# Kernel tuning notes

Hardware: AMD Instinct MI355X
Metric: run time of the kernel (lower is better)

Reference implementation:

```python
import jax, jax.numpy as jnp
import numpy as np

B, S, D = 64, 256, 512          # batch, seq_len_max, num_dim (= in_dim = nclass)
H, DO = 8, 64                   # num_heads, out_dim per head (H*DO == D)
ALPHA = 0.2                     # leaky_relu negative slope
N = B * S                       # nodes
DEG = 32
E = N * DEG + N                 # random edges + self-loops


def setup_inputs() -> dict:
    key = jax.random.key(0)
    k = jax.random.split(key, 7)
    h = jax.random.normal(k[0], (B, S, D), jnp.float32)
    loops = jnp.arange(N, dtype=jnp.int32)
    src = jnp.concatenate([jax.random.randint(k[1], (N * DEG,), 0, N, jnp.int32), loops])
    dst = jnp.concatenate([jax.random.randint(k[2], (N * DEG,), 0, N, jnp.int32), loops])
    W1 = jax.random.normal(k[3], (H, D, DO), jnp.float32) * 0.05      # per-head fc weight
    a1 = jax.random.normal(k[4], (H, 2 * DO), jnp.float32) * 0.05     # per-head attn_fc weight
    Wout = jax.random.normal(k[5], (H * DO, D), jnp.float32) * 0.05   # out_att fc
    aout = jax.random.normal(k[6], (2 * D,), jnp.float32) * 0.05      # out_att attn_fc
    return {"h": h, "W1": W1, "a1": a1, "Wout": Wout, "aout": aout, "src": src, "dst": dst}


def gat_head(x, W, a, src, dst, concat):
    # x: [N, in_d], W: [in_d, d], a: [2d]
    z = x @ W                                   # [N, d]
    d = W.shape[1]
    es = z @ a[:d]                              # src part of attn score, [N]
    ed = z @ a[d:]                              # dst part, [N]
    e = jax.nn.leaky_relu(es[src] + ed[dst], ALPHA)   # [E]
    # segment softmax over incoming edges of each dst node
    m = jax.ops.segment_max(e, dst, num_segments=N)
    m = jnp.where(jnp.isfinite(m), m, 0.0)
    ex = jnp.exp(e - m[dst])
    den = jax.ops.segment_sum(ex, dst, num_segments=N)
    att = ex / den[dst]                         # [E] (self-loops guarantee den > 0)
    out = jax.ops.segment_sum(att[:, None] * z[src], dst, num_segments=N)  # [N, d]
    return jax.nn.elu(out) if concat else out


def reference(h, W1, a1, Wout, aout, src, dst):
    x = h.reshape(N, D)                         # dropout is identity at eval
    heads = jax.vmap(lambda W, a: gat_head(x, W, a, src, dst, True))(W1, a1)  # [H, N, DO]
    hcat = jnp.transpose(heads, (1, 0, 2)).reshape(N, H * DO)                 # [N, H*DO]
    out = jax.nn.elu(gat_head(hcat, Wout, aout, src, dst, False))             # [N, D]
    return (out + x).reshape(B, S, D)
```

## Files before the change

kernel.cpp:

```cpp
#include <hip/hip_runtime.h>
#include <stdint.h>

#define DD 512
#define HH 8
#define DOO 64
#define ALPHA 0.2f

typedef __attribute__((ext_vector_type(8))) short short8;
typedef __attribute__((ext_vector_type(4))) float floatx4;
typedef __attribute__((ext_vector_type(4))) unsigned short u16x4;
typedef unsigned short u16;

static __device__ __forceinline__ float bf2f(u16 u){
  union { unsigned int u; float f; } c; c.u = ((unsigned int)u) << 16; return c.f;
}
static __device__ __forceinline__ u16 f2bf(float f){
  union { float f; unsigned int u; } c; c.f = f;
  unsigned int u = c.u;
  unsigned int r = (u + 0x7FFFu + ((u >> 16) & 1u)) >> 16;
  return (u16)r;
}
static __device__ __forceinline__ float leaky(float s){ return (s >= 0.f) ? s : ALPHA * s; }
static __device__ __forceinline__ float elu(float v){ return (v > 0.f) ? v : (__expf(v) - 1.f); }

#define PERM_LO 0x01000504u
#define PERM_HI 0x03020706u

#define DOT2(accv, pairv, wv) \
  asm("v_dot2_f32_bf16 %0, %1, %2, %0" : "+v"(accv) : "v"(pairv), "v"(wv))

#define DOTS8(ZA, ZB, AQ) do{ unsigned pr_; \
  pr_=__builtin_amdgcn_perm((ZA).x,(ZB).x,PERM_LO); DOT2(acc[0],pr_,(AQ)); \
  pr_=__builtin_amdgcn_perm((ZA).x,(ZB).x,PERM_HI); DOT2(acc[1],pr_,(AQ)); \
  pr_=__builtin_amdgcn_perm((ZA).y,(ZB).y,PERM_LO); DOT2(acc[2],pr_,(AQ)); \
  pr_=__builtin_amdgcn_perm((ZA).y,(ZB).y,PERM_HI); DOT2(acc[3],pr_,(AQ)); \
  pr_=__builtin_amdgcn_perm((ZA).z,(ZB).z,PERM_LO); DOT2(acc[4],pr_,(AQ)); \
  pr_=__builtin_amdgcn_perm((ZA).z,(ZB).z,PERM_HI); DOT2(acc[5],pr_,(AQ)); \
  pr_=__builtin_amdgcn_perm((ZA).w,(ZB).w,PERM_LO); DOT2(acc[6],pr_,(AQ)); \
  pr_=__builtin_amdgcn_perm((ZA).w,(ZB).w,PERM_HI); DOT2(acc[7],pr_,(AQ)); \
}while(0)

#define GLOAD_LDS16(g, l) \
  __builtin_amdgcn_global_load_lds((const __attribute__((address_space(1))) void*)(g), \
                                   (__attribute__((address_space(3))) void*)(l), 16, 0, 0)

__global__ void k_prep(const float* __restrict__ h, u16* __restrict__ xb,
                       const float* __restrict__ W1, u16* __restrict__ wbt1,
                       const float* __restrict__ Wout, u16* __restrict__ wbt2,
                       const int* __restrict__ dst, int* deg,
                       int n4, int E){
  int i = blockIdx.x * blockDim.x + threadIdx.x;
  if (i < n4){
    float4 v = ((const float4*)h)[i];
    u16x4 o;
    o[0] = f2bf(v.x); o[1] = f2bf(v.y); o[2] = f2bf(v.z); o[3] = f2bf(v.w);
    ((u16x4*)xb)[i] = o;
    return;
  }
  i -= n4;
  if (i < HH * DD * DOO / 8){
    int idx0 = i * 8;
    #pragma unroll
    for (int t = 0; t < 8; t++){
      int idx = idx0 + t;
      int hh = idx >> 15;
      int rem = idx & 32767;
      int k = rem >> 6;
      int dd = rem & 63;
      wbt1[(hh * 64 + dd) * DD + k] = f2bf(W1[idx]);
    }
    return;
  }
  i -= HH * DD * DOO / 8;
  if (i < DD * DD){
    int k = i >> 9, n = i & 511;
    wbt2[n * DD + k] = f2bf(Wout[i]);
    return;
  }
  i -= DD * DD;
  if (i < E) atomicAdd(&deg[dst[i]], 1);
}

__global__ void k_scan(const int* __restrict__ deg, int* __restrict__ off, int N){
  __shared__ int sm[1024];
  int tid = threadIdx.x;
  const int per = 16;
  int base = tid * per;
  int loc[per];
  int t = 0;
  #pragma unroll
  for (int i = 0; i < per; i++){
    int v = (base + i < N) ? deg[base + i] : 0;
    v = (v + 1) & ~1;
    loc[i] = v; t += v;
  }
  sm[tid] = t; __syncthreads();
  for (int o = 1; o < 1024; o <<= 1){
    int v = 0;
    if (tid >= o) v = sm[tid - o];
    __syncthreads();
    sm[tid] += v;
    __syncthreads();
  }
  int run = sm[tid] - t;
  #pragma unroll
  for (int i = 0; i < per; i++){ if (base + i < N) off[base + i] = run; run += loc[i]; }
  if (tid == 1023) off[N] = run;
}

__global__ void k_scatter(const int* __restrict__ src, const int* __restrict__ dst,
                          const int* __restrict__ off, int* cursor, int* __restrict__ csr, int E){
  int i = blockIdx.x * blockDim.x + threadIdx.x;
  if (i < E){
    int d = dst[i];
    int p = atomicAdd(&cursor[d], 1);
    csr[off[d] + p] = src[i];
  }
}

__global__ __launch_bounds__(256) void k_gemm(const u16* __restrict__ A,
                                              const u16* __restrict__ BT,
                                              u16* __restrict__ C, int M){
  __shared__ __attribute__((aligned(16))) u16 As[128 * 64];
  __shared__ __attribute__((aligned(16))) u16 Bs[128 * 64];
  const int tid = threadIdx.x;
  const int wid = tid >> 6, lane = tid & 63;
  const int n0 = blockIdx.x * 128, m0 = blockIdx.y * 128;
  const int wr = wid >> 1, wc = wid & 1;
  const int row16 = lane & 15, kg = lane >> 4;
  floatx4 acc[4][4];
  #pragma unroll
  for (int i = 0; i < 4; i++)
    #pragma unroll
    for (int j = 0; j < 4; j++) acc[i][j] = (floatx4)0.0f;

  for (int kt = 0; kt < DD; kt += 64){
    #pragma unroll
    for (int i = 0; i < 4; i++){
      int chunk = i * 256 + tid;
      int m = chunk >> 3, g = chunk & 7;
      int gs = g ^ (m & 7);
      GLOAD_LDS16(A + (size_t)(m0 + m) * DD + kt + gs * 8, &As[chunk * 8]);
      GLOAD_LDS16(BT + (size_t)(n0 + m) * DD + kt + gs * 8, &Bs[chunk * 8]);
    }
    __syncthreads();
    short8 af[4][2], bf[4][2];
    #pragma unroll
    for (int mi = 0; mi < 4; mi++)
      #pragma unroll
      for (int kk = 0; kk < 2; kk++){
        int row = wr * 64 + mi * 16 + row16;
        int gr = (kk * 4 + kg) ^ (row & 7);
        af[mi][kk] = *(const short8*)(&As[(row * 8 + gr) * 8]);
      }
    #pragma unroll
    for (int ni = 0; ni < 4; ni++)
      #pragma unroll
      for (int kk = 0; kk < 2; kk++){
        int row = wc * 64 + ni * 16 + row16;
        int gr = (kk * 4 + kg) ^ (row & 7);
        bf[ni][kk] = *(const short8*)(&Bs[(row * 8 + gr) * 8]);
      }
    #pragma unroll
    for (int kk = 0; kk < 2; kk++)
      #pragma unroll
      for (int mi = 0; mi < 4; mi++)
        #pragma unroll
        for (int ni = 0; ni < 4; ni++)
          acc[mi][ni] = __builtin_amdgcn_mfma_f32_16x16x32_bf16(af[mi][kk], bf[ni][kk], acc[mi][ni], 0, 0, 0);
    __syncthreads();
  }
  #pragma unroll
  for (int mi = 0; mi < 4; mi++)
    #pragma unroll
    for (int ni = 0; ni < 4; ni++)
      #pragma unroll
      for (int j = 0; j < 4; j++){
        int r = m0 + wr * 64 + mi * 16 + kg * 4 + j;
        int c = n0 + wc * 64 + ni * 16 + row16;
        C[(size_t)r * DD + c] = f2bf(acc[mi][ni][j]);
      }
}

__global__ void k_scores1(const u16* __restrict__ z, const float* __restrict__ a1,
                          float* __restrict__ es, float* __restrict__ ed, int N){
  int wid = threadIdx.x >> 6, lane = threadIdx.x & 63;
  int n = blockIdx.x * 4 + wid;
  if (n >= N) return;
  int h = lane >> 3, j8 = lane & 7;
  short8 zv = *(const short8*)(z + (size_t)n * DD + lane * 8);
  float esv = 0.f, edv = 0.f;
  #pragma unroll
  for (int t = 0; t < 8; t++){
    float f = bf2f((u16)zv[t]);
    esv += f * a1[h * 128 + j8 * 8 + t];
    edv += f * a1[h * 128 + 64 + j8 * 8 + t];
  }
  #pragma unroll
  for (int d2 = 1; d2 < 8; d2 <<= 1){ esv += __shfl_xor(esv, d2); edv += __shfl_xor(edv, d2); }
  if (j8 == 0){ es[n * 8 + h] = esv; ed[n * 8 + h] = edv; }
}

__global__ void k_scores2(const u16* __restrict__ z, const float* __restrict__ aout,
                          float* __restrict__ es, float* __restrict__ ed, int N){
  int wid = threadIdx.x >> 6, lane = threadIdx.x & 63;
  int n = blockIdx.x * 4 + wid;
  if (n >= N) return;
  short8 zv = *(const short8*)(z + (size_t)n * DD + lane * 8);
  float esv = 0.f, edv = 0.f;
  #pragma unroll
  for (int t = 0; t < 8; t++){
    float f = bf2f((u16)zv[t]);
    esv += f * aout[lane * 8 + t];
    edv += f * aout[512 + lane * 8 + t];
  }
  #pragma unroll
  for (int d2 = 1; d2 < 64; d2 <<= 1){ esv += __shfl_xor(esv, d2); edv += __shfl_xor(edv, d2); }
  if (lane == 0){ es[n] = esv; ed[n] = edv; }
}

__global__ void k_edgew1(const float* __restrict__ es, const float* __restrict__ ed,
                         const int* __restrict__ off, const int* __restrict__ deg,
                         int* __restrict__ csr, unsigned* __restrict__ wp,
                         float* __restrict__ den1, int N, int ep2){
  int wid = threadIdx.x >> 6, lane = threadIdx.x & 63;
  int n = blockIdx.x * 4 + wid;
  if (n >= N) return;
  int o0 = off[n], cntp = off[n + 1] - o0, cnt = deg[n];
  float edh[8];
  {
    float4 d0 = *(const float4*)(ed + (size_t)n * 8);
    float4 d1 = *(const float4*)(ed + (size_t)n * 8 + 4);
    edh[0]=d0.x; edh[1]=d0.y; edh[2]=d0.z; edh[3]=d0.w;
    edh[4]=d1.x; edh[5]=d1.y; edh[6]=d1.z; edh[7]=d1.w;
  }
  float den[8];
  #pragma unroll
  for (int h = 0; h < 8; h++) den[h] = 0.f;
  for (int base = 0; base < cntp; base += 64){
    int e = base + lane;
    float wv[8];
    if (e < cnt){
      int s = csr[o0 + e];
      float4 e0 = *(const float4*)(es + (size_t)s * 8);
      float4 e1 = *(const float4*)(es + (size_t)s * 8 + 4);
      float ev[8] = {e0.x, e0.y, e0.z, e0.w, e1.x, e1.y, e1.z, e1.w};
      #pragma unroll
      for (int h = 0; h < 8; h++){
        float w = __expf(leaky(ev[h] + edh[h]));
        wv[h] = w; den[h] += w;
      }
    } else {
      if (e < cntp) csr[o0 + e] = 0;
      #pragma unroll
      for (int h = 0; h < 8; h++) wv[h] = 0.f;
    }
    #pragma unroll
    for (int h = 0; h < 8; h++){
      float wn = __shfl_down(wv[h], 1);
      if (!(lane & 1) && e < cntp){
        unsigned pk;
        asm("v_cvt_pk_bf16_f32 %0, %1, %2" : "=v"(pk) : "v"(wv[h]), "v"(wn));
        wp[(size_t)h * ep2 + ((o0 + e) >> 1)] = pk;
      }
    }
  }
  #pragma unroll
  for (int h = 0; h < 8; h++){
    float d = den[h];
    #pragma unroll
    for (int d2 = 1; d2 < 64; d2 <<= 1) d += __shfl_xor(d, d2);
    if (lane == 0) den1[(size_t)n * 8 + h] = d;
  }
}

__global__ void k_edgew2(const float* __restrict__ es, const float* __restrict__ ed,
                         const int* __restrict__ off, const int* __restrict__ deg,
                         int* __restrict__ csr, unsigned* __restrict__ wp,
                         float* __restrict__ den2, int N){
  int wid = threadIdx.x >> 6, lane = threadIdx.x & 63;
  int n = blockIdx.x * 4 + wid;
  if (n >= N) return;
  int o0 = off[n], cntp = off[n + 1] - o0, cnt = deg[n];
  float edn = ed[n];
  float dsum = 0.f;
  for (int base = 0; base < cntp; base += 64){
    int e = base + lane;
    float w = 0.f;
    if (e < cnt){
      int s = csr[o0 + e];
      w = __expf(leaky(es[s] + edn));
      dsum += w;
    } else if (e < cntp){
      csr[o0 + e] = 0;
    }
    float wn = __shfl_down(w, 1);
    if (!(lane & 1) && e < cntp){
      unsigned pk;
      asm("v_cvt_pk_bf16_f32 %0, %1, %2" : "=v"(pk) : "v"(w), "v"(wn));
      wp[(o0 + e) >> 1] = pk;
    }
  }
  #pragma unroll
  for (int d2 = 1; d2 < 64; d2 <<= 1) dsum += __shfl_xor(dsum, d2);
  if (lane == 0) den2[n] = dsum;
}

__global__ __launch_bounds__(256) void k_agg1(const u16* __restrict__ z,
    const unsigned* __restrict__ wp, const float* __restrict__ den1,
    const int* __restrict__ off, const int* __restrict__ csr,
    u16* __restrict__ hcat, int N, int ep2){
  int wid = threadIdx.x >> 6, lane = threadIdx.x & 63;
  int n = blockIdx.x * 4 + wid;
  if (n >= N) return;
  int p = blockIdx.y;
  int o0 = off[n];
  int npairs = (off[n + 1] - o0) >> 1;
  int qb = o0 >> 1;
  int g = lane >> 4, li = lane & 15;
  int head = 2 * p + (li >> 3);
  const unsigned* wph = wp + (size_t)head * ep2 + qb;
  const int2* cp = (const int2*)csr + qb;
  int coloff = p * 128 + li * 8;
  const u16* zc = z + coloff;
  float acc[8];
  #pragma unroll
  for (int j = 0; j < 8; j++) acc[j] = 0.f;

  uint4 zA0 = {0,0,0,0}, zA1 = {0,0,0,0}, zB0 = {0,0,0,0}, zB1 = {0,0,0,0};
  unsigned aqA = 0, aqB = 0;
  {
    int q0 = g, q1 = 4 + g;
    if (q0 < npairs){
      int2 sp = cp[q0]; aqA = wph[q0];
      zA0 = *(const uint4*)(zc + (size_t)sp.x * DD);
      zA1 = *(const uint4*)(zc + (size_t)sp.y * DD);
    }
    if (q1 < npairs){
      int2 sp = cp[q1]; aqB = wph[q1];
      zB0 = *(const uint4*)(zc + (size_t)sp.x * DD);
      zB1 = *(const uint4*)(zc + (size_t)sp.y * DD);
    }
  }
  int itn = (npairs + 3) >> 2;
  for (int it = 2; it < itn + 2; it += 2){
    int q2 = it * 4 + g, q3 = q2 + 4;
    bool v2 = q2 < npairs, v3 = q3 < npairs;
    int2 sp2 = {0,0}, sp3 = {0,0};
    unsigned naqA = 0, naqB = 0;
    if (v2){ sp2 = cp[q2]; naqA = wph[q2]; }
    if (v3){ sp3 = cp[q3]; naqB = wph[q3]; }
    DOTS8(zA0, zA1, aqA);
    uint4 nzA0 = {0,0,0,0}, nzA1 = {0,0,0,0};
    if (v2){
      nzA0 = *(const uint4*)(zc + (size_t)sp2.x * DD);
      nzA1 = *(const uint4*)(zc + (size_t)sp2.y * DD);
    }
    DOTS8(zB0, zB1, aqB);
    uint4 nzB0 = {0,0,0,0}, nzB1 = {0,0,0,0};
    if (v3){
      nzB0 = *(const uint4*)(zc + (size_t)sp3.x * DD);
      nzB1 = *(const uint4*)(zc + (size_t)sp3.y * DD);
    }
    zA0 = nzA0; zA1 = nzA1; aqA = naqA;
    zB0 = nzB0; zB1 = nzB1; aqB = naqB;
  }
  #pragma unroll
  for (int j = 0; j < 8; j++){
    acc[j] += __shfl_xor(acc[j], 16);
    acc[j] += __shfl_xor(acc[j], 32);
  }
  if (lane < 16){
    float inv = 1.f / den1[(size_t)n * 8 + head];
    short8 o;
    #pragma unroll
    for (int j = 0; j < 8; j++) o[j] = (short)f2bf(elu(acc[j] * inv));
    *(short8*)(hcat + (size_t)n * DD + coloff) = o;
  }
}

__global__ __launch_bounds__(256) void k_agg2(const u16* __restrict__ z,
    const unsigned* __restrict__ wp, const float* __restrict__ den2,
    const int* __restrict__ off, const int* __restrict__ csr,
    const u16* __restrict__ xb, float* __restrict__ out, int N){
  int wid = threadIdx.x >> 6, lane = threadIdx.x & 63;
  int n = blockIdx.x * 4 + wid;
  if (n >= N) return;
  int p = blockIdx.y;
  int o0 = off[n];
  int npairs = (off[n + 1] - o0) >> 1;
  int qb = o0 >> 1;
  int g = lane >> 4, li = lane & 15;
  const unsigned* wph = wp + qb;
  const int2* cp = (const int2*)csr + qb;
  int coloff = p * 128 + li * 8;
  const u16* zc = z + coloff;
  float acc[8];
  #pragma unroll
  for (int j = 0; j < 8; j++) acc[j] = 0.f;

  uint4 zA0 = {0,0,0,0}, zA1 = {0,0,0,0}, zB0 = {0,0,0,0}, zB1 = {0,0,0,0};
  unsigned aqA = 0, aqB = 0;
  {
    int q0 = g, q1 = 4 + g;
    if (q0 < npairs){
      int2 sp = cp[q0]; aqA = wph[q0];
      zA0 = *(const uint4*)(zc + (size_t)sp.x * DD);
      zA1 = *(const uint4*)(zc + (size_t)sp.y * DD);
    }
    if (q1 < npairs){
      int2 sp = cp[q1]; aqB = wph[q1];
      zB0 = *(const uint4*)(zc + (size_t)sp.x * DD);
      zB1 = *(const uint4*)(zc + (size_t)sp.y * DD);
    }
  }
  int itn = (npairs + 3) >> 2;
  for (int it = 2; it < itn + 2; it += 2){
    int q2 = it * 4 + g, q3 = q2 + 4;
    bool v2 = q2 < npairs, v3 = q3 < npairs;
    int2 sp2 = {0,0}, sp3 = {0,0};
    unsigned naqA = 0, naqB = 0;
    if (v2){ sp2 = cp[q2]; naqA = wph[q2]; }
    if (v3){ sp3 = cp[q3]; naqB = wph[q3]; }
    DOTS8(zA0, zA1, aqA);
    uint4 nzA0 = {0,0,0,0}, nzA1 = {0,0,0,0};
    if (v2){
      nzA0 = *(const uint4*)(zc + (size_t)sp2.x * DD);
      nzA1 = *(const uint4*)(zc + (size_t)sp2.y * DD);
    }
    DOTS8(zB0, zB1, aqB);
    uint4 nzB0 = {0,0,0,0}, nzB1 = {0,0,0,0};
    if (v3){
      nzB0 = *(const uint4*)(zc + (size_t)sp3.x * DD);
      nzB1 = *(const uint4*)(zc + (size_t)sp3.y * DD);
    }
    zA0 = nzA0; zA1 = nzA1; aqA = naqA;
    zB0 = nzB0; zB1 = nzB1; aqB = naqB;
  }
  #pragma unroll
  for (int j = 0; j < 8; j++){
    acc[j] += __shfl_xor(acc[j], 16);
    acc[j] += __shfl_xor(acc[j], 32);
  }
  if (lane < 16){
    float inv = 1.f / den2[n];
    short8 xv = *(const short8*)(xb + (size_t)n * DD + coloff);
    float ov[8];
    #pragma unroll
    for (int j = 0; j < 8; j++) ov[j] = elu(acc[j] * inv) + bf2f((u16)xv[j]);
    float4 o0v, o1v;
    o0v.x = ov[0]; o0v.y = ov[1]; o0v.z = ov[2]; o0v.w = ov[3];
    o1v.x = ov[4]; o1v.y = ov[5]; o1v.z = ov[6]; o1v.w = ov[7];
    *(float4*)(out + (size_t)n * DD + coloff) = o0v;
    *(float4*)(out + (size_t)n * DD + coloff + 4) = o1v;
  }
}

extern "C" void kernel_launch(void* const* d_in, const int* in_sizes, int n_in,
                              void* d_out, int out_size, void* d_ws, size_t ws_size,
                              hipStream_t stream){
  const float* h   = (const float*)d_in[0];
  const float* W1  = (const float*)d_in[1];
  const float* a1  = (const float*)d_in[2];
  const float* Wout= (const float*)d_in[3];
  const float* aout= (const float*)d_in[4];
  const int* src   = (const int*)d_in[5];
  const int* dst   = (const int*)d_in[6];
  float* out = (float*)d_out;
  const int N = in_sizes[0] / DD;
  const int E = in_sizes[5];
  const int EP = E + N;
  const int ep2 = EP >> 1;

  char* p = (char*)d_ws;
  auto alloc = [&](size_t bytes) -> char* {
    char* r = p;
    p += (bytes + 255) & ~(size_t)255;
    return r;
  };
  u16* xb    = (u16*)alloc((size_t)N * DD * 2);
  u16* z1b   = (u16*)alloc((size_t)N * DD * 2);
  u16* hcat  = (u16*)alloc((size_t)N * DD * 2);
  u16* wbt1  = (u16*)alloc((size_t)DD * DD * 2);
  u16* wbt2  = (u16*)alloc((size_t)DD * DD * 2);
  float* es1 = (float*)alloc((size_t)N * HH * 4);
  float* ed1 = (float*)alloc((size_t)N * HH * 4);
  float* es2 = (float*)alloc((size_t)N * 4);
  float* ed2 = (float*)alloc((size_t)N * 4);
  float* den1= (float*)alloc((size_t)N * HH * 4);
  float* den2= (float*)alloc((size_t)N * 4);
  int* deg   = (int*)alloc((size_t)N * 4);
  int* off   = (int*)alloc((size_t)(N + 1) * 4);
  int* cursor= (int*)alloc((size_t)N * 4);
  int* csr   = (int*)alloc((size_t)EP * 4);
  unsigned* wp1 = (unsigned*)alloc((size_t)HH * ep2 * 4);
  unsigned* wp2 = (unsigned*)alloc((size_t)ep2 * 4);

  hipMemsetAsync(deg, 0, (size_t)((char*)csr - (char*)deg), stream);

  int n4 = N * DD / 4;
  int prep_threads = n4 + HH * DD * DOO / 8 + DD * DD + E;
  k_prep<<<(prep_threads + 255) / 256, 256, 0, stream>>>(h, xb, W1, wbt1, Wout, wbt2, dst, deg, n4, E);
  k_scan<<<1, 1024, 0, stream>>>(deg, off, N);
  k_scatter<<<(E + 255) / 256, 256, 0, stream>>>(src, dst, off, cursor, csr, E);

  dim3 gg(DD / 128, N / 128);
  dim3 ga((N + 3) / 4, 4);
  dim3 gw((N + 3) / 4);

  k_gemm<<<gg, 256, 0, stream>>>(xb, wbt1, z1b, N);
  k_scores1<<<(N + 3) / 4, 256, 0, stream>>>(z1b, a1, es1, ed1, N);
  k_edgew1<<<gw, 256, 0, stream>>>(es1, ed1, off, deg, csr, wp1, den1, N, ep2);
  k_agg1<<<ga, 256, 0, stream>>>(z1b, wp1, den1, off, csr, hcat, N, ep2);

  k_gemm<<<gg, 256, 0, stream>>>(hcat, wbt2, z1b, N);
  k_scores2<<<(N + 3) / 4, 256, 0, stream>>>(z1b, aout, es2, ed2, N);
  k_edgew2<<<gw, 256, 0, stream>>>(es2, ed2, off, deg, csr, wp2, den2, N);
  k_agg2<<<ga, 256, 0, stream>>>(z1b, wp2, den2, off, csr, xb, out, N);
}
```

Before: 250.0 us.

## Restructure aggregation kernels to one wave per node over full row width

The aggregation kernels now use one wavefront per destination node, with each lane covering 8 of the 512 columns. This replaces the previous 4-way column split across blockIdx.y and the cross-lane shuffle reduction. CSR segments are padded to multiples of 4 so each iteration loads edge indices with a single int4 and needs no bounds checks. Layer-1 edge weights switch to edge-major interleaved heads so each pair of edges is written as two 16-byte stores. The cost is one extra padded edge per node on average and reads of index entries past the last segment, which are zeroed in the scatter kernel.

```diff
diff --git a/kernel.cpp b/kernel.cpp
--- a/kernel.cpp
+++ b/kernel.cpp
@@ -43,6 +43,10 @@
 #define GLOAD_LDS16(g, l) \
   __builtin_amdgcn_global_load_lds((const __attribute__((address_space(1))) void*)(g), \
                                    (__attribute__((address_space(3))) void*)(l), 16, 0, 0)
+
+static __device__ __forceinline__ uint4 rowl(const u16* __restrict__ zp, int s, int lane){
+  return ((const uint4*)(zp + ((size_t)(unsigned)s << 9)))[lane];
+}
 
 __global__ void k_prep(const float* __restrict__ h, u16* __restrict__ xb,
                        const float* __restrict__ W1, u16* __restrict__ wbt1,
@@ -91,7 +95,7 @@
   #pragma unroll
   for (int i = 0; i < per; i++){
     int v = (base + i < N) ? deg[base + i] : 0;
-    v = (v + 1) & ~1;
+    v = (v + 3) & ~3;
     loc[i] = v; t += v;
   }
   sm[tid] = t; __syncthreads();
@@ -109,8 +113,12 @@
 }
 
 __global__ void k_scatter(const int* __restrict__ src, const int* __restrict__ dst,
-                          const int* __restrict__ off, int* cursor, int* __restrict__ csr, int E){
+                          const int* __restrict__ off, int* cursor, int* __restrict__ csr,
+                          int E, int N){
   int i = blockIdx.x * blockDim.x + threadIdx.x;
+  if (i < 256){
+    csr[off[N] + i] = 0;
+  }
   if (i < E){
     int d = dst[i];
     int p = atomicAdd(&cursor[d], 1);
@@ -222,7 +230,7 @@
 __global__ void k_edgew1(const float* __restrict__ es, const float* __restrict__ ed,
                          const int* __restrict__ off, const int* __restrict__ deg,
                          int* __restrict__ csr, unsigned* __restrict__ wp,
-                         float* __restrict__ den1, int N, int ep2){
+                         float* __restrict__ den1, int N){
   int wid = threadIdx.x >> 6, lane = threadIdx.x & 63;
   int n = blockIdx.x * 4 + wid;
   if (n >= N) return;
@@ -255,14 +263,18 @@
       #pragma unroll
       for (int h = 0; h < 8; h++) wv[h] = 0.f;
     }
+    unsigned pk[8];
     #pragma unroll
     for (int h = 0; h < 8; h++){
       float wn = __shfl_down(wv[h], 1);
-      if (!(lane & 1) && e < cntp){
-        unsigned pk;
-        asm("v_cvt_pk_bf16_f32 %0, %1, %2" : "=v"(pk) : "v"(wv[h]), "v"(wn));
-        wp[(size_t)h * ep2 + ((o0 + e) >> 1)] = pk;
-      }
+      asm("v_cvt_pk_bf16_f32 %0, %1, %2" : "=v"(pk[h]) : "v"(wv[h]), "v"(wn));
+    }
+    if (!(lane & 1) && e < cntp){
+      size_t q = (size_t)((o0 + e) >> 1) * 8;
+      uint4 v0; v0.x = pk[0]; v0.y = pk[1]; v0.z = pk[2]; v0.w = pk[3];
+      uint4 v1; v1.x = pk[4]; v1.y = pk[5]; v1.z = pk[6]; v1.w = pk[7];
+      *(uint4*)(wp + q) = v0;
+      *(uint4*)(wp + q + 4) = v1;
     }
   }
   #pragma unroll
@@ -309,151 +321,96 @@
 __global__ __launch_bounds__(256) void k_agg1(const u16* __restrict__ z,
     const unsigned* __restrict__ wp, const float* __restrict__ den1,
     const int* __restrict__ off, const int* __restrict__ csr,
-    u16* __restrict__ hcat, int N, int ep2){
-  int wid = threadIdx.x >> 6, lane = threadIdx.x & 63;
-  int n = blockIdx.x * 4 + wid;
-  if (n >= N) return;
-  int p = blockIdx.y;
+    u16* __restrict__ hcat, int N){
+  int wid = __builtin_amdgcn_readfirstlane(threadIdx.x >> 6);
+  int lane = threadIdx.x & 63;
+  int n = blockIdx.x * 4 + wid;
+  if (n >= N) return;
   int o0 = off[n];
-  int npairs = (off[n + 1] - o0) >> 1;
-  int qb = o0 >> 1;
-  int g = lane >> 4, li = lane & 15;
-  int head = 2 * p + (li >> 3);
-  const unsigned* wph = wp + (size_t)head * ep2 + qb;
-  const int2* cp = (const int2*)csr + qb;
-  int coloff = p * 128 + li * 8;
-  const u16* zc = z + coloff;
+  int itn = (off[n + 1] - o0) >> 2;
+  const int4* cp4 = (const int4*)(csr + o0);
+  int pb = o0 >> 1;
+  int head = lane >> 3;
+  const unsigned* wpb = wp + (size_t)pb * 8 + head;
   float acc[8];
   #pragma unroll
   for (int j = 0; j < 8; j++) acc[j] = 0.f;
 
-  uint4 zA0 = {0,0,0,0}, zA1 = {0,0,0,0}, zB0 = {0,0,0,0}, zB1 = {0,0,0,0};
-  unsigned aqA = 0, aqB = 0;
+  uint4 zA0, zA1, zB0, zB1;
+  unsigned aqA, aqB;
+  int4 c1;
   {
-    int q0 = g, q1 = 4 + g;
-    if (q0 < npairs){
-      int2 sp = cp[q0]; aqA = wph[q0];
-      zA0 = *(const uint4*)(zc + (size_t)sp.x * DD);
-      zA1 = *(const uint4*)(zc + (size_t)sp.y * DD);
-    }
-    if (q1 < npairs){
-      int2 sp = cp[q1]; aqB = wph[q1];
-      zB0 = *(const uint4*)(zc + (size_t)sp.x * DD);
-      zB1 = *(const uint4*)(zc + (size_t)sp.y * DD);
-    }
-  }
-  int itn = (npairs + 3) >> 2;
-  for (int it = 2; it < itn + 2; it += 2){
-    int q2 = it * 4 + g, q3 = q2 + 4;
-    bool v2 = q2 < npairs, v3 = q3 < npairs;
-    int2 sp2 = {0,0}, sp3 = {0,0};
-    unsigned naqA = 0, naqB = 0;
-    if (v2){ sp2 = cp[q2]; naqA = wph[q2]; }
-    if (v3){ sp3 = cp[q3]; naqB = wph[q3]; }
+    int4 c0 = cp4[0];
+    c1 = cp4[1];
+    zA0 = rowl(z, c0.x, lane); zA1 = rowl(z, c0.y, lane);
+    zB0 = rowl(z, c0.z, lane); zB1 = rowl(z, c0.w, lane);
+    aqA = wpb[0]; aqB = wpb[8];
+  }
+  for (int it = 0; it < itn; ++it){
+    int4 cn = cp4[it + 2];
+    uint4 nA0 = rowl(z, c1.x, lane), nA1 = rowl(z, c1.y, lane);
+    uint4 nB0 = rowl(z, c1.z, lane), nB1 = rowl(z, c1.w, lane);
+    unsigned naqA = wpb[(size_t)(2 * it + 2) * 8];
+    unsigned naqB = wpb[(size_t)(2 * it + 3) * 8];
     DOTS8(zA0, zA1, aqA);
-    uint4 nzA0 = {0,0,0,0}, nzA1 = {0,0,0,0};
-    if (v2){
-      nzA0 = *(const uint4*)(zc + (size_t)sp2.x * DD);
-      nzA1 = *(const uint4*)(zc + (size_t)sp2.y * DD);
-    }
     DOTS8(zB0, zB1, aqB);
-    uint4 nzB0 = {0,0,0,0}, nzB1 = {0,0,0,0};
-    if (v3){
-      nzB0 = *(const uint4*)(zc + (size_t)sp3.x * DD);
-      nzB1 = *(const uint4*)(zc + (size_t)sp3.y * DD);
-    }
-    zA0 = nzA0; zA1 = nzA1; aqA = naqA;
-    zB0 = nzB0; zB1 = nzB1; aqB = naqB;
-  }
-  #pragma unroll
-  for (int j = 0; j < 8; j++){
-    acc[j] += __shfl_xor(acc[j], 16);
-    acc[j] += __shfl_xor(acc[j], 32);
-  }
-  if (lane < 16){
-    float inv = 1.f / den1[(size_t)n * 8 + head];
-    short8 o;
-    #pragma unroll
-    for (int j = 0; j < 8; j++) o[j] = (short)f2bf(elu(acc[j] * inv));
-    *(short8*)(hcat + (size_t)n * DD + coloff) = o;
-  }
+    zA0 = nA0; zA1 = nA1; zB0 = nB0; zB1 = nB1;
+    aqA = naqA; aqB = naqB; c1 = cn;
+  }
+  float inv = 1.f / den1[(size_t)n * 8 + head];
+  short8 o;
+  #pragma unroll
+  for (int j = 0; j < 8; j++) o[j] = (short)f2bf(elu(acc[j] * inv));
+  *(short8*)(hcat + (size_t)n * DD + lane * 8) = o;
 }
 
 __global__ __launch_bounds__(256) void k_agg2(const u16* __restrict__ z,
     const unsigned* __restrict__ wp, const float* __restrict__ den2,
     const int* __restrict__ off, const int* __restrict__ csr,
     const u16* __restrict__ xb, float* __restrict__ out, int N){
-  int wid = threadIdx.x >> 6, lane = threadIdx.x & 63;
-  int n = blockIdx.x * 4 + wid;
-  if (n >= N) return;
-  int p = blockIdx.y;
+  int wid = __builtin_amdgcn_readfirstlane(threadIdx.x >> 6);
+  int lane = threadIdx.x & 63;
+  int n = blockIdx.x * 4 + wid;
+  if (n >= N) return;
   int o0 = off[n];
-  int npairs = (off[n + 1] - o0) >> 1;
-  int qb = o0 >> 1;
-  int g = lane >> 4, li = lane & 15;
-  const unsigned* wph = wp + qb;
-  const int2* cp = (const int2*)csr + qb;
-  int coloff = p * 128 + li * 8;
-  const u16* zc = z + coloff;
+  int itn = (off[n + 1] - o0) >> 2;
+  const int4* cp4 = (const int4*)(csr + o0);
+  int pb = o0 >> 1;
   float acc[8];
   #pragma unroll
   for (int j = 0; j < 8; j++) acc[j] = 0.f;
 
-  uint4 zA0 = {0,0,0,0}, zA1 = {0,0,0,0}, zB0 = {0,0,0,0}, zB1 = {0,0,0,0};
-  unsigned aqA = 0, aqB = 0;
+  uint4 zA0, zA1, zB0, zB1;
+  unsigned aqA, aqB;
+  int4 c1;
   {
-    int q0 = g, q1 = 4 + g;
-    if (q0 < npairs){
-      int2 sp = cp[q0]; aqA = wph[q0];
-      zA0 = *(const uint4*)(zc + (size_t)sp.x * DD);
-      zA1 = *(const uint4*)(zc + (size_t)sp.y * DD);
-    }
-    if (q1 < npairs){
-      int2 sp = cp[q1]; aqB = wph[q1];
-      zB0 = *(const uint4*)(zc + (size_t)sp.x * DD);
-      zB1 = *(const uint4*)(zc + (size_t)sp.y * DD);
-    }
-  }
-  int itn = (npairs + 3) >> 2;
-  for (int it = 2; it < itn + 2; it += 2){
-    int q2 = it * 4 + g, q3 = q2 + 4;
-    bool v2 = q2 < npairs, v3 = q3 < npairs;
-    int2 sp2 = {0,0}, sp3 = {0,0};
-    unsigned naqA = 0, naqB = 0;
-    if (v2){ sp2 = cp[q2]; naqA = wph[q2]; }
-    if (v3){ sp3 = cp[q3]; naqB = wph[q3]; }
+    int4 c0 = cp4[0];
+    c1 = cp4[1];
+    zA0 = rowl(z, c0.x, lane); zA1 = rowl(z, c0.y, lane);
+    zB0 = rowl(z, c0.z, lane); zB1 = rowl(z, c0.w, lane);
+    uint2 a01 = *(const uint2*)(wp + pb);
+    aqA = a01.x; aqB = a01.y;
+  }
+  for (int it = 0; it < itn; ++it){
+    int4 cn = cp4[it + 2];
+    uint4 nA0 = rowl(z, c1.x, lane), nA1 = rowl(z, c1.y, lane);
+    uint4 nB0 = rowl(z, c1.z, lane), nB1 = rowl(z, c1.w, lane);
+    uint2 an = *(const uint2*)(wp + pb + 2 * it + 2);
     DOTS8(zA0, zA1, aqA);
-    uint4 nzA0 = {0,0,0,0}, nzA1 = {0,0,0,0};
-    if (v2){
-      nzA0 = *(const uint4*)(zc + (size_t)sp2.x * DD);
-      nzA1 = *(const uint4*)(zc + (size_t)sp2.y * DD);
-    }
     DOTS8(zB0, zB1, aqB);
-    uint4 nzB0 = {0,0,0,0}, nzB1 = {0,0,0,0};
-    if (v3){
-      nzB0 = *(const uint4*)(zc + (size_t)sp3.x * DD);
-      nzB1 = *(const uint4*)(zc + (size_t)sp3.y * DD);
-    }
-    zA0 = nzA0; zA1 = nzA1; aqA = naqA;
-    zB0 = nzB0; zB1 = nzB1; aqB = naqB;
-  }
-  #pragma unroll
-  for (int j = 0; j < 8; j++){
-    acc[j] += __shfl_xor(acc[j], 16);
-    acc[j] += __shfl_xor(acc[j], 32);
-  }
-  if (lane < 16){
-    float inv = 1.f / den2[n];
-    short8 xv = *(const short8*)(xb + (size_t)n * DD + coloff);
-    float ov[8];
-    #pragma unroll
-    for (int j = 0; j < 8; j++) ov[j] = elu(acc[j] * inv) + bf2f((u16)xv[j]);
-    float4 o0v, o1v;
-    o0v.x = ov[0]; o0v.y = ov[1]; o0v.z = ov[2]; o0v.w = ov[3];
-    o1v.x = ov[4]; o1v.y = ov[5]; o1v.z = ov[6]; o1v.w = ov[7];
-    *(float4*)(out + (size_t)n * DD + coloff) = o0v;
-    *(float4*)(out + (size_t)n * DD + coloff + 4) = o1v;
-  }
+    zA0 = nA0; zA1 = nA1; zB0 = nB0; zB1 = nB1;
+    aqA = an.x; aqB = an.y; c1 = cn;
+  }
+  float inv = 1.f / den2[n];
+  short8 xv = *(const short8*)(xb + (size_t)n * DD + lane * 8);
+  float ov[8];
+  #pragma unroll
+  for (int j = 0; j < 8; j++) ov[j] = elu(acc[j] * inv) + bf2f((u16)xv[j]);
+  float4 o0v, o1v;
+  o0v.x = ov[0]; o0v.y = ov[1]; o0v.z = ov[2]; o0v.w = ov[3];
+  o1v.x = ov[4]; o1v.y = ov[5]; o1v.z = ov[6]; o1v.w = ov[7];
+  *(float4*)(out + (size_t)n * DD + lane * 8) = o0v;
+  *(float4*)(out + (size_t)n * DD + lane * 8 + 4) = o1v;
 }
 
 extern "C" void kernel_launch(void* const* d_in, const int* in_sizes, int n_in,
@@ -469,7 +426,7 @@
   float* out = (float*)d_out;
   const int N = in_sizes[0] / DD;
   const int E = in_sizes[5];
-  const int EP = E + N;
+  const int EP = E + 3 * N + 512;
   const int ep2 = EP >> 1;
 
   char* p = (char*)d_ws;
@@ -493,8 +450,8 @@
   int* off   = (int*)alloc((size_t)(N + 1) * 4);
   int* cursor= (int*)alloc((size_t)N * 4);
   int* csr   = (int*)alloc((size_t)EP * 4);
-  unsigned* wp1 = (unsigned*)alloc((size_t)HH * ep2 * 4);
-  unsigned* wp2 = (unsigned*)alloc((size_t)ep2 * 4);
+  unsigned* wp1 = (unsigned*)alloc(((size_t)ep2 * 8 + 64) * 4);
+  unsigned* wp2 = (unsigned*)alloc(((size_t)ep2 + 64) * 4);
 
   hipMemsetAsync(deg, 0, (size_t)((char*)csr - (char*)deg), stream);
 
@@ -502,19 +459,18 @@
   int prep_threads = n4 + HH * DD * DOO / 8 + DD * DD + E;
   k_prep<<<(prep_threads + 255) / 256, 256, 0, stream>>>(h, xb, W1, wbt1, Wout, wbt2, dst, deg, n4, E);
   k_scan<<<1, 1024, 0, stream>>>(deg, off, N);
-  k_scatter<<<(E + 255) / 256, 256, 0, stream>>>(src, dst, off, cursor, csr, E);
+  k_scatter<<<(E + 255) / 256, 256, 0, stream>>>(src, dst, off, cursor, csr, E, N);
 
   dim3 gg(DD / 128, N / 128);
-  dim3 ga((N + 3) / 4, 4);
-  dim3 gw((N + 3) / 4);
+  dim3 ga((N + 3) / 4);
 
   k_gemm<<<gg, 256, 0, stream>>>(xb, wbt1, z1b, N);
   k_scores1<<<(N + 3) / 4, 256, 0, stream>>>(z1b, a1, es1, ed1, N);
-  k_edgew1<<<gw, 256, 0, stream>>>(es1, ed1, off, deg, csr, wp1, den1, N, ep2);
-  k_agg1<<<ga, 256, 0, stream>>>(z1b, wp1, den1, off, csr, hcat, N, ep2);
+  k_edgew1<<<ga, 256, 0, stream>>>(es1, ed1, off, deg, csr, wp1, den1, N);
+  k_agg1<<<ga, 256, 0, stream>>>(z1b, wp1, den1, off, csr, hcat, N);
 
   k_gemm<<<gg, 256, 0, stream>>>(hcat, wbt2, z1b, N);
   k_scores2<<<(N + 3) / 4, 256, 0, stream>>>(z1b, aout, es2, ed2, N);
-  k_edgew2<<<gw, 256, 0, stream>>>(es2, ed2, off, deg, csr, wp2, den2, N);
+  k_edgew2<<<ga, 256, 0, stream>>>(es2, ed2, off, deg, csr, wp2, den2, N);
   k_agg2<<<ga, 256, 0, stream>>>(z1b, wp2, den2, off, csr, xb, out, N);
 }
```

Result: slower. 281.3 us (+12.5%).
